# Performance work log

Hardware: AMD Instinct MI355X
Metric: run time of the kernel (lower is better)

## Reference

```python
import jax, jax.numpy as jnp
import numpy as np

B, S, HID = 2, 2048, 1024
H, KV, D = 16, 8, 64
NDIM = 2          # position_ids.shape[-1]
EPS = 1e-6
SCALING = 1.0


def _rms_norm(x, w=None, eps=EPS):
    # matches _RMSNorm: fp32 compute, optional learnable scale
    xf = x.astype(jnp.float32)
    n = xf * jax.lax.rsqrt(jnp.mean(xf * xf, axis=-1, keepdims=True) + eps)
    if w is not None:
        n = n * w.astype(jnp.float32)
    return n.astype(x.dtype)


def _rotate_half(x):
    d = x.shape[-1] // 2
    return jnp.concatenate([-x[..., d:], x[..., :d]], axis=-1)


def _apply_multidim_rope(x, cos, sin, ndim):
    # x: [B,S,h,D]; cos/sin: [B,S,D]; unsqueeze_dim=2 broadcasts over heads
    num_channels = x.shape[-1]
    cpd = 2 * (num_channels // (2 * ndim))  # channels per RoPE dimension
    outs = []
    for k in range(ndim):
        sl = slice(k * cpd, (k + 1) * cpd)
        xk = x[..., sl]
        ck = cos[..., sl][:, :, None, :]
        sk = sin[..., sl][:, :, None, :]
        outs.append(xk * ck + _rotate_half(xk) * sk)
    return jnp.concatenate(outs, axis=-1)


def setup_inputs() -> dict:
    key = jax.random.key(0)
    ks = jax.random.split(key, 10)
    scale = 0.02
    return {
        "hidden_states": jax.random.normal(ks[0], (B, S, HID), jnp.float32),
        "cos": jax.random.normal(ks[1], (B, S, D), jnp.float32),
        "sin": jax.random.normal(ks[2], (B, S, D), jnp.float32),
        "position_ids": jax.random.randint(ks[3], (B, S, NDIM), 0, 64, jnp.int64),
        "Wq": jax.random.normal(ks[4], (HID, H * D), jnp.float32) * scale,
        "Wk": jax.random.normal(ks[5], (HID, KV * D), jnp.float32) * scale,
        "Wv": jax.random.normal(ks[6], (HID, KV * D), jnp.float32) * scale,
        "Wo": jax.random.normal(ks[7], (H * D, HID), jnp.float32) * scale,
        "q_norm_w": jnp.ones((D,), jnp.float32),
        "k_norm_w": jnp.ones((D,), jnp.float32),
    }


def reference(hidden_states, cos, sin, position_ids, Wq, Wk, Wv, Wo, q_norm_w, k_norm_w):
    ndim = position_ids.shape[-1]
    bsz, seq_len, _ = hidden_states.shape

    q = (hidden_states @ Wq).reshape(bsz, seq_len, H, D)
    q = _rms_norm(q, q_norm_w)
    q = _apply_multidim_rope(q, cos, sin, ndim)
    q = jnp.transpose(q, (0, 2, 1, 3))  # [B,H,S,D]

    k = (hidden_states @ Wk).reshape(bsz, seq_len, KV, D)
    k = _rms_norm(k, k_norm_w)
    k = _apply_multidim_rope(k, cos, sin, ndim)
    k = jnp.transpose(k, (0, 2, 1, 3))  # [B,KV,S,D]

    v = (hidden_states @ Wv).reshape(bsz, seq_len, KV, D)
    v = _rms_norm(v, None)  # v_norm has no scale
    v = jnp.transpose(v, (0, 2, 1, 3))  # [B,KV,S,D]

    groups = H // KV
    if groups > 1:
        k = jnp.repeat(k, groups, axis=1)  # [B,H,S,D]
        v = jnp.repeat(v, groups, axis=1)

    scores = jnp.einsum("bhqd,bhkd->bhqk", q, k) * SCALING
    attn = jax.nn.softmax(scores.astype(jnp.float32), axis=-1).astype(q.dtype)
    out = jnp.einsum("bhqk,bhkd->bhqd", attn, v)
    out = jnp.transpose(out, (0, 2, 1, 3)).reshape(bsz, seq_len, H * D)
    return out @ Wo
```

## Files before the change

kernel.cpp:

```cpp
#include <hip/hip_runtime.h>

#define PB 2
#define PS 2048
#define PHID 1024
#define PH 16
#define PKV 8
#define PD 64
#define PM (PB*PS)
#define PR (PB*PH*PS)

typedef _Float16 f16_t;
typedef _Float16 f16x8 __attribute__((ext_vector_type(8)));
typedef _Float16 f16x2 __attribute__((ext_vector_type(2)));
typedef __fp16 fp16v2 __attribute__((ext_vector_type(2)));
typedef float f32x4 __attribute__((ext_vector_type(4)));

#define MFMAH(a,b,c)  __builtin_amdgcn_mfma_f32_16x16x32_f16((a),(b),(c),0,0,0)
#define LOG2E 1.44269504f

__device__ __forceinline__ void gl16(const f16_t* g, f16_t* l) {
  __builtin_amdgcn_global_load_lds(
      (const __attribute__((address_space(1))) void*)g,
      (__attribute__((address_space(3))) void*)l, 16, 0, 0);
}

__global__ __launch_bounds__(256)
void convert_all(const float* __restrict__ hs,
                 const float* __restrict__ Wq, const float* __restrict__ Wk,
                 const float* __restrict__ Wv, const float* __restrict__ Wo,
                 f16_t* __restrict__ hf, f16_t* __restrict__ wtT)
{
  __shared__ float Tt[64][68];
  const int tid = threadIdx.x;

  if (blockIdx.x < 2048) {
    const size_t i = ((size_t)blockIdx.x * 256 + tid) * 8;
    float4 a = *(const float4*)&hs[i];
    float4 b = *(const float4*)&hs[i + 4];
    float xs[8] = {a.x, a.y, a.z, a.w, b.x, b.y, b.z, b.w};
    f16x8 v;
    #pragma unroll
    for (int j = 0; j < 8; ++j) v[j] = (f16_t)xs[j];
    *(f16x8*)&hf[i] = v;
    return;
  }

  const int wb = blockIdx.x - 2048;
  const int slot = wb >> 4, k0 = (wb & 15) * 64;

  const float* src; int N, ncol0, orow0;
  if (slot < 16)      { src = Wq; N = 1024; ncol0 = slot*64;      orow0 = slot*64; }
  else if (slot < 24) { src = Wk; N = 512;  ncol0 = (slot-16)*64; orow0 = 1024 + (slot-16)*64; }
  else if (slot < 32) { src = Wv; N = 512;  ncol0 = (slot-24)*64; orow0 = 1536 + (slot-24)*64; }
  else                { src = Wo; N = 1024; ncol0 = (slot-32)*64; orow0 = 2048 + (slot-32)*64; }

  const int tk = tid >> 6, tn = tid & 63;
  #pragma unroll
  for (int i = 0; i < 16; ++i)
    Tt[tn][tk*16 + i] = src[(size_t)(k0 + tk*16 + i) * N + ncol0 + tn];
  __syncthreads();

  const int n = tid >> 2, kc = (tid & 3) * 16;
  f16x8 a0, a1;
  #pragma unroll
  for (int i = 0; i < 8; ++i) {
    a0[i] = (f16_t)Tt[n][kc + i];
    a1[i] = (f16_t)Tt[n][kc + 8 + i];
  }
  const size_t ob = (size_t)(orow0 + n) * 1024 + k0 + kc;
  *(f16x8*)&wtT[ob]     = a0;
  *(f16x8*)&wtT[ob + 8] = a1;
}

__global__ __launch_bounds__(256)
void qkv_kernel(const f16_t* __restrict__ hsf, const f16_t* __restrict__ wtT,
                const float* __restrict__ cosp, const float* __restrict__ sinp,
                const float* __restrict__ qnw, const float* __restrict__ knw,
                f16_t* __restrict__ q_o, f16_t* __restrict__ k_o,
                f16_t* __restrict__ vt_o)
{
  __shared__ __align__(16) f16_t Ah[128][64];
  __shared__ __align__(16) f16_t Bh[128][64];

  const int tid = threadIdx.x;
  const int lane = tid & 63, wave = tid >> 6;
  const int lo16 = lane & 15, hi4 = lane >> 4;
  const int lin = blockIdx.x;
  const int swz = (lin & 7) * 64 + (lin >> 3);
  const int m0 = (swz >> 4) * 128;
  const int ws = swz & 15;
  const int orow = ws * 128;

  int kind, hd0;
  if (ws < 8)       { kind = 0; hd0 = ws*2; }
  else if (ws < 12) { kind = 1; hd0 = (ws-8)*2; }
  else              { kind = 2; hd0 = (ws-12)*2; }

  f32x4 acc[2][8];
  #pragma unroll
  for (int qb = 0; qb < 2; ++qb)
    #pragma unroll
    for (int j = 0; j < 8; ++j) acc[qb][j] = f32x4{0.f, 0.f, 0.f, 0.f};

  const int ri = lane >> 3, pc = lane & 7;
  const int lcs = (pc ^ ri) * 8;
  size_t aoff4[4]; f16_t* aldst4[4];
  size_t boff4[4]; f16_t* bldst4[4];
  #pragma unroll
  for (int q = 0; q < 4; ++q) {
    aoff4[q] = (size_t)(m0 + wave*32 + q*8 + ri) * PHID + lcs;
    aldst4[q] = &Ah[wave*32 + q*8][0];
    boff4[q] = (size_t)(orow + wave*32 + q*8 + ri) * 1024 + lcs;
    bldst4[q] = &Bh[wave*32 + q*8][0];
  }

  const int rsw = lo16 & 7;

  for (int k0 = 0; k0 < PHID; k0 += 64) {
    __syncthreads();
    #pragma unroll
    for (int q = 0; q < 4; ++q) gl16(hsf + aoff4[q] + k0, aldst4[q]);
    #pragma unroll
    for (int q = 0; q < 4; ++q) gl16(wtT + boff4[q] + k0, bldst4[q]);
    __syncthreads();

    #pragma unroll
    for (int t = 0; t < 2; ++t) {
      const int ccol = ((t*4 + hi4) ^ rsw) * 8;
      f16x8 ah[2];
      #pragma unroll
      for (int qb = 0; qb < 2; ++qb)
        ah[qb] = *(const f16x8*)&Ah[wave*32 + qb*16 + lo16][ccol];
      #pragma unroll
      for (int j = 0; j < 8; ++j) {
        f16x8 bh = *(const f16x8*)&Bh[j*16 + lo16][ccol];
        #pragma unroll
        for (int qb = 0; qb < 2; ++qb)
          acc[qb][j] = MFMAH(ah[qb], bh, acc[qb][j]);
      }
    }
  }

  float nwv[4];
  #pragma unroll
  for (int jj = 0; jj < 4; ++jj)
    nwv[jj] = (kind == 0) ? qnw[lo16 + 16*jj]
            : (kind == 1) ? knw[lo16 + 16*jj] : 1.0f;

  #pragma unroll
  for (int qb = 0; qb < 2; ++qb) {
    float sc[2][4];
    #pragma unroll
    for (int r = 0; r < 4; ++r) {
      float s0 = 0.f, s1 = 0.f;
      #pragma unroll
      for (int j = 0; j < 4; ++j) {
        s0 += acc[qb][j][r]   * acc[qb][j][r];
        s1 += acc[qb][j+4][r] * acc[qb][j+4][r];
      }
      #pragma unroll
      for (int m = 1; m < 16; m <<= 1) {
        s0 += __shfl_xor(s0, m);
        s1 += __shfl_xor(s1, m);
      }
      sc[0][r] = 1.0f / sqrtf(s0 * (1.0f/64.0f) + 1e-6f);
      sc[1][r] = 1.0f / sqrtf(s1 * (1.0f/64.0f) + 1e-6f);
    }

    float y[8][4];
    #pragma unroll
    for (int j = 0; j < 8; ++j)
      #pragma unroll
      for (int r = 0; r < 4; ++r)
        y[j][r] = acc[qb][j][r] * sc[j>>2][r] * nwv[j&3];

    if (kind == 2) {
      #pragma unroll
      for (int r = 0; r < 4; ++r) {
        int mg = m0 + wave*32 + qb*16 + hi4*4 + r;
        int b = mg >> 11, sq = mg & 2047;
        int g = sq & 63;
        int sp = (g & 3) | (((g >> 4) & 1) << 2) | (((g >> 2) & 1) << 3)
               | (((g >> 3) & 1) << 4) | (g & 32);
        int sq2 = (sq & ~63) | sp;
        #pragma unroll
        for (int j = 0; j < 8; ++j) {
          int d = lo16 + 16*(j & 3), hd = hd0 + (j >> 2);
          vt_o[((size_t)((b*PKV + hd)*PD + d))*PS + sq2] = (f16_t)y[j][r];
        }
      }
    } else {
      #pragma unroll
      for (int r = 0; r < 4; ++r) {
        int mg = m0 + wave*32 + qb*16 + hi4*4 + r;
        int b = mg >> 11, sq = mg & 2047;
        const float* cp = &cosp[(size_t)mg * PD];
        const float* sp = &sinp[(size_t)mg * PD];
        float z[8];
        #pragma unroll
        for (int j = 0; j < 8; ++j) {
          int d = lo16 + 16*(j & 3);
          float c = cp[d], s = sp[d];
          float rot = (j & 1) ? y[j-1][r] : -y[j+1][r];
          z[j] = y[j][r] * c + rot * s;
        }
        #pragma unroll
        for (int j = 0; j < 8; ++j) {
          int d = lo16 + 16*(j & 3), hd = hd0 + (j >> 2);
          if (kind == 0) {
            size_t idx = ((size_t)(b*PH + hd)*PS + sq)*PD + d;
            q_o[idx] = (f16_t)(z[j] * LOG2E);
          } else {
            size_t idx = ((size_t)(b*PKV + hd)*PS + sq)*PD + d;
            k_o[idx] = (f16_t)z[j];
          }
        }
      }
    }
  }
}

__global__ __launch_bounds__(512, 4)
void attn_kernel(const f16_t* __restrict__ q_g, const f16_t* __restrict__ k_g,
                 const f16_t* __restrict__ vt_g,
                 f16_t* __restrict__ op, float2* __restrict__ ml)
{
  __shared__ __align__(16) char lds_raw[32768];
  f16_t (*Ks)[64][64] = (f16_t (*)[64][64])lds_raw;
  f16_t (*Vs)[64][64] = (f16_t (*)[64][64])(lds_raw + 16384);
  f16_t (*Ob)[72]     = (f16_t (*)[72])lds_raw;

  const int tid = threadIdx.x, lane = tid & 63, wave = tid >> 6;
  const int lo16 = lane & 15, hi4 = lane >> 4;
  const int lin = blockIdx.x;
  const int swz = (lin & 7) * 64 + (lin >> 3);
  const int qt = swz & 7;
  const int bh = (swz >> 3) & 31;
  const int ks = swz >> 8;
  const int b = bh >> 4, h = bh & 15, kvh = h >> 1;

  f16x8 qf[2][2];
  #pragma unroll
  for (int qb = 0; qb < 2; ++qb) {
    const size_t qbase = ((size_t)(b*PH + h)*PS + qt*256 + wave*32 + qb*16 + lo16) * PD;
    #pragma unroll
    for (int t = 0; t < 2; ++t)
      qf[qb][t] = *(const f16x8*)&q_g[qbase + t*32 + hi4*8];
  }

  f32x4 o[2][4];
  float mq[2] = {0.f, 0.f}, lq[2] = {0.f, 0.f};
  #pragma unroll
  for (int qb = 0; qb < 2; ++qb)
    #pragma unroll
    for (int j = 0; j < 4; ++j) o[qb][j] = f32x4{0.f, 0.f, 0.f, 0.f};

  const int ri = lane >> 3;
  const int lcs = ((lane & 7) ^ ri) * 8;
  const size_t kbase = (size_t)(b*PKV + kvh) * PS * PD + (size_t)ks * 1024 * PD;
  const size_t vbase = (size_t)(b*PKV + kvh) * PD * PS + (size_t)ks * 1024;

  auto STAGE = [&](int kt, int buf) {
    const f16_t* kp = k_g + kbase + (size_t)kt * 64 * PD;
    const f16_t* vp = vt_g + vbase + kt * 64;
    const int st = wave;
    gl16(kp + (st*8 + ri)*PD + lcs, &Ks[buf][st*8][0]);
    gl16(vp + (size_t)(st*8 + ri)*PS + lcs, &Vs[buf][st*8][0]);
  };

  STAGE(0, 0);
  int cur = 0;
  const int rsw = lo16 & 7;

  for (int kt = 0; kt < 16; ++kt) {
    __syncthreads();
    if (kt + 1 < 16) STAGE(kt + 1, cur ^ 1);

    f32x4 sacc[2][4];
    __builtin_amdgcn_s_setprio(1);
    #pragma unroll
    for (int j = 0; j < 4; ++j) {
      f16x8 kf0 = *(const f16x8*)&Ks[cur][j*16 + lo16][(hi4 ^ rsw) * 8];
      f16x8 kf1 = *(const f16x8*)&Ks[cur][j*16 + lo16][((4 + hi4) ^ rsw) * 8];
      #pragma unroll
      for (int qb = 0; qb < 2; ++qb) {
        const f32x4 mc = {-mq[qb], -mq[qb], -mq[qb], -mq[qb]};
        sacc[qb][j] = MFMAH(kf1, qf[qb][1], MFMAH(kf0, qf[qb][0], mc));
      }
    }
    __builtin_amdgcn_s_setprio(0);

    f16x8 pa[2][2];
    #pragma unroll
    for (int qb = 0; qb < 2; ++qb) {
      float x0 = fmaxf(fmaxf(sacc[qb][0][0], sacc[qb][0][1]),
                       fmaxf(sacc[qb][0][2], sacc[qb][0][3]));
      float x1 = fmaxf(fmaxf(sacc[qb][1][0], sacc[qb][1][1]),
                       fmaxf(sacc[qb][1][2], sacc[qb][1][3]));
      float x2 = fmaxf(fmaxf(sacc[qb][2][0], sacc[qb][2][1]),
                       fmaxf(sacc[qb][2][2], sacc[qb][2][3]));
      float x3 = fmaxf(fmaxf(sacc[qb][3][0], sacc[qb][3][1]),
                       fmaxf(sacc[qb][3][2], sacc[qb][3][3]));
      float tm = fmaxf(fmaxf(x0, x1), fmaxf(x2, x3));
      tm = fmaxf(tm, __shfl_xor(tm, 16));
      tm = fmaxf(tm, __shfl_xor(tm, 32));

      float ls = 0.f;
      if (!__all(tm <= 8.0f)) {
        float tmx = fmaxf(tm, 0.f);
        float alpha = __builtin_amdgcn_exp2f(-tmx);
        lq[qb] *= alpha;
        #pragma unroll
        for (int jd = 0; jd < 4; ++jd) o[qb][jd] *= alpha;
        mq[qb] += tmx;
        #pragma unroll
        for (int t = 0; t < 2; ++t) {
          union { fp16v2 h[4]; f16x8 v; } u;
          #pragma unroll
          for (int pr = 0; pr < 4; ++pr) {
            float p0 = __builtin_amdgcn_exp2f(sacc[qb][2*t + (pr>>1)][(pr&1)*2]     - tmx);
            float p1 = __builtin_amdgcn_exp2f(sacc[qb][2*t + (pr>>1)][(pr&1)*2 + 1] - tmx);
            ls += p0 + p1;
            u.h[pr] = __builtin_amdgcn_cvt_pkrtz(p0, p1);
          }
          pa[qb][t] = u.v;
        }
      } else {
        #pragma unroll
        for (int t = 0; t < 2; ++t) {
          union { fp16v2 h[4]; f16x8 v; } u;
          #pragma unroll
          for (int pr = 0; pr < 4; ++pr) {
            float p0 = __builtin_amdgcn_exp2f(sacc[qb][2*t + (pr>>1)][(pr&1)*2]);
            float p1 = __builtin_amdgcn_exp2f(sacc[qb][2*t + (pr>>1)][(pr&1)*2 + 1]);
            ls += p0 + p1;
            u.h[pr] = __builtin_amdgcn_cvt_pkrtz(p0, p1);
          }
          pa[qb][t] = u.v;
        }
      }
      lq[qb] += ls;
    }

    __builtin_amdgcn_s_setprio(1);
    #pragma unroll
    for (int jd = 0; jd < 4; ++jd) {
      #pragma unroll
      for (int t = 0; t < 2; ++t) {
        f16x8 vf = *(const f16x8*)&Vs[cur][jd*16 + lo16][((t*4 + hi4) ^ rsw) * 8];
        #pragma unroll
        for (int qb = 0; qb < 2; ++qb)
          o[qb][jd] = MFMAH(vf, pa[qb][t], o[qb][jd]);
      }
    }
    __builtin_amdgcn_s_setprio(0);

    cur ^= 1;
  }

  #pragma unroll
  for (int qb = 0; qb < 2; ++qb) {
    lq[qb] += __shfl_xor(lq[qb], 16);
    lq[qb] += __shfl_xor(lq[qb], 32);
  }
  __syncthreads();
  const int rbase = bh*PS + qt*256 + wave*32;
  if (hi4 == 0) {
    #pragma unroll
    for (int qb = 0; qb < 2; ++qb)
      ml[(size_t)ks*PR + rbase + qb*16 + lo16] = float2{mq[qb], lq[qb]};
  }
  const int wl = wave & 3;
  #pragma unroll
  for (int pass = 0; pass < 2; ++pass) {
    if ((wave >> 2) == pass) {
      #pragma unroll
      for (int qb = 0; qb < 2; ++qb) {
        float inv = 1.0f / lq[qb];
        #pragma unroll
        for (int jd = 0; jd < 4; ++jd)
          #pragma unroll
          for (int rp = 0; rp < 2; ++rp)
            *(f16x2*)&Ob[wl*32 + qb*16 + lo16][jd*16 + hi4*4 + 2*rp] =
                f16x2{(f16_t)(o[qb][jd][2*rp] * inv), (f16_t)(o[qb][jd][2*rp+1] * inv)};
      }
      const int row = lane >> 1, half = lane & 1;
      const size_t gb_ = ((size_t)ks*PR + rbase + row) * PD + half*32;
      #pragma unroll
      for (int c = 0; c < 4; ++c)
        *(f16x8*)&op[gb_ + c*8] = *(const f16x8*)&Ob[wl*32 + row][half*32 + c*8];
    }
    __syncthreads();
  }
}

__global__ __launch_bounds__(256)
void merge_kernel(const f16_t* __restrict__ op, const float2* __restrict__ ml,
                  f16_t* __restrict__ ao)
{
  const int gid = blockIdx.x * 256 + threadIdx.x;
  const int row = gid >> 3, oct = gid & 7;
  float2 e0 = ml[row], e1 = ml[PR + row];
  float M = fmaxf(e0.x, e1.x);
  float c0 = __builtin_amdgcn_exp2f(e0.x - M) * e0.y;
  float c1 = __builtin_amdgcn_exp2f(e1.x - M) * e1.y;
  float inv = 1.0f / (c0 + c1);
  c0 *= inv; c1 *= inv;
  f16x8 a = *(const f16x8*)&op[(size_t)row*PD + oct*8];
  f16x8 bq = *(const f16x8*)&op[(size_t)(PR + row)*PD + oct*8];
  f16x8 r;
  #pragma unroll
  for (int i = 0; i < 8; ++i)
    r[i] = (f16_t)(c0 * (float)a[i] + c1 * (float)bq[i]);
  const int bh = row >> 11, sq = row & 2047;
  const int b = bh >> 4, h = bh & 15;
  *(f16x8*)&ao[((size_t)(b*PS + sq))*PHID + h*PD + oct*8] = r;
}

__global__ __launch_bounds__(256)
void oproj_kernel(const f16_t* __restrict__ ao, const f16_t* __restrict__ woT,
                  float* __restrict__ out)
{
  __shared__ __align__(16) f16_t As[128][64];
  __shared__ __align__(16) f16_t Bs[64][64];

  const int tid = threadIdx.x;
  const int lane = tid & 63, wave = tid >> 6;
  const int lo16 = lane & 15, hi4 = lane >> 4;
  const int lin = blockIdx.x;
  const int swz = (lin & 7) * 64 + (lin >> 3);
  const int m0 = (swz >> 4) * 128;
  const int col0 = (swz & 15) * 64;

  f32x4 acc[2][4];
  #pragma unroll
  for (int qb = 0; qb < 2; ++qb)
    #pragma unroll
    for (int j = 0; j < 4; ++j) acc[qb][j] = f32x4{0.f, 0.f, 0.f, 0.f};

  const int ri = lane >> 3, pc = lane & 7;
  const int lcs = (pc ^ ri) * 8;
  size_t aoff4[4]; f16_t* aldst4[4];
  #pragma unroll
  for (int q = 0; q < 4; ++q) {
    aoff4[q] = (size_t)(m0 + wave*32 + q*8 + ri) * PHID + lcs;
    aldst4[q] = &As[wave*32 + q*8][0];
  }
  size_t boff[2]; int brow[2];
  #pragma unroll
  for (int q = 0; q < 2; ++q) {
    brow[q] = wave*16 + q*8;
    boff[q] = (size_t)(col0 + brow[q] + ri) * 1024 + lcs;
  }

  const int rsw = lo16 & 7;

  for (int k0 = 0; k0 < PHID; k0 += 64) {
    __syncthreads();
    #pragma unroll
    for (int q = 0; q < 4; ++q) gl16(ao + aoff4[q] + k0, aldst4[q]);
    #pragma unroll
    for (int q = 0; q < 2; ++q) gl16(woT + boff[q] + k0, &Bs[brow[q]][0]);
    __syncthreads();

    #pragma unroll
    for (int t = 0; t < 2; ++t) {
      const int ccol = ((t*4 + hi4) ^ rsw) * 8;
      f16x8 a[2];
      #pragma unroll
      for (int qb = 0; qb < 2; ++qb)
        a[qb] = *(const f16x8*)&As[wave*32 + qb*16 + lo16][ccol];
      #pragma unroll
      for (int j = 0; j < 4; ++j) {
        f16x8 bb = *(const f16x8*)&Bs[j*16 + lo16][ccol];
        #pragma unroll
        for (int qb = 0; qb < 2; ++qb)
          acc[qb][j] = MFMAH(a[qb], bb, acc[qb][j]);
      }
    }
  }

  #pragma unroll
  for (int qb = 0; qb < 2; ++qb)
    #pragma unroll
    for (int r = 0; r < 4; ++r) {
      int mg = m0 + wave*32 + qb*16 + hi4*4 + r;
      #pragma unroll
      for (int j = 0; j < 4; ++j)
        out[(size_t)mg*PHID + col0 + lo16 + 16*j] = acc[qb][j][r];
    }
}

extern "C" void kernel_launch(void* const* d_in, const int* in_sizes, int n_in,
                              void* d_out, int out_size, void* d_ws, size_t ws_size,
                              hipStream_t stream) {
  (void)in_sizes; (void)n_in; (void)out_size; (void)ws_size;
  const float* hs   = (const float*)d_in[0];
  const float* cosp = (const float*)d_in[1];
  const float* sinp = (const float*)d_in[2];
  const float* Wq   = (const float*)d_in[4];
  const float* Wk   = (const float*)d_in[5];
  const float* Wv   = (const float*)d_in[6];
  const float* Wo   = (const float*)d_in[7];
  const float* qnw  = (const float*)d_in[8];
  const float* knw  = (const float*)d_in[9];
  float* out = (float*)d_out;

  const size_t QN = (size_t)PB*PH*PS*PD;
  const size_t KN = (size_t)PB*PKV*PS*PD;
  const size_t HN = (size_t)PM*PHID;
  char* wsb = (char*)d_ws;
  f16_t*  qv  = (f16_t*)wsb;
  f16_t*  kv  = qv + QN;
  f16_t*  vt  = kv + KN;
  f16_t*  hsf = vt + KN;
  f16_t*  wtT = hsf + HN;
  f16_t*  op  = wtT + (size_t)3072*1024;
  float2* ml  = (float2*)(op + 2*QN);
  f16_t*  ao  = qv;
  const f16_t* woT = wtT + (size_t)2048*1024;

  convert_all<<<dim3(2816), 256, 0, stream>>>(hs, Wq, Wk, Wv, Wo, hsf, wtT);
  qkv_kernel<<<dim3(512),  256, 0, stream>>>(hsf, wtT, cosp, sinp,
                                             qnw, knw, qv, kv, vt);
  attn_kernel<<<dim3(512), 512, 0, stream>>>(qv, kv, vt, op, ml);
  merge_kernel<<<dim3(PR*8/256), 256, 0, stream>>>(op, ml, ao);
  oproj_kernel<<<dim3(512), 256, 0, stream>>>(ao, woT, out);
}
```

Baseline: 113.9 us.

## Fuse hidden-state fp16 conversion into QKV GEMM and split-merge into O-projection

The QKV GEMM now reads fp32 hidden states directly, converts them to fp16 in registers, and prefetches the next tile with register loads instead of using a separate conversion pass. The split-K attention merge is folded into the O-projection A-tile load, with a small kernel that precomputes only the per-row combine weights. This removes two full intermediate tensor round-trips through global memory and one kernel's worth of traffic. In exchange, the GEMM A loads become synchronous register loads plus conversion work, and oproj does redundant merge arithmetic across the 16 column blocks that share each row.

Result: slower. 135.3 us (+18.8%).

```diff
diff --git a/kernel.cpp b/kernel.cpp
--- a/kernel.cpp
+++ b/kernel.cpp
@@ -25,28 +25,13 @@
 }
 
 __global__ __launch_bounds__(256)
-void convert_all(const float* __restrict__ hs,
-                 const float* __restrict__ Wq, const float* __restrict__ Wk,
-                 const float* __restrict__ Wv, const float* __restrict__ Wo,
-                 f16_t* __restrict__ hf, f16_t* __restrict__ wtT)
+void convert_w(const float* __restrict__ Wq, const float* __restrict__ Wk,
+               const float* __restrict__ Wv, const float* __restrict__ Wo,
+               f16_t* __restrict__ wtT)
 {
   __shared__ float Tt[64][68];
   const int tid = threadIdx.x;
-
-  if (blockIdx.x < 2048) {
-    const size_t i = ((size_t)blockIdx.x * 256 + tid) * 8;
-    float4 a = *(const float4*)&hs[i];
-    float4 b = *(const float4*)&hs[i + 4];
-    float xs[8] = {a.x, a.y, a.z, a.w, b.x, b.y, b.z, b.w};
-    f16x8 v;
-    #pragma unroll
-    for (int j = 0; j < 8; ++j) v[j] = (f16_t)xs[j];
-    *(f16x8*)&hf[i] = v;
-    return;
-  }
-
-  const int wb = blockIdx.x - 2048;
-  const int slot = wb >> 4, k0 = (wb & 15) * 64;
+  const int slot = blockIdx.x >> 4, k0 = (blockIdx.x & 15) * 64;
 
   const float* src; int N, ncol0, orow0;
   if (slot < 16)      { src = Wq; N = 1024; ncol0 = slot*64;      orow0 = slot*64; }
@@ -73,7 +58,7 @@
 }
 
 __global__ __launch_bounds__(256)
-void qkv_kernel(const f16_t* __restrict__ hsf, const f16_t* __restrict__ wtT,
+void qkv_kernel(const float* __restrict__ hs, const f16_t* __restrict__ wtT,
                 const float* __restrict__ cosp, const float* __restrict__ sinp,
                 const float* __restrict__ qnw, const float* __restrict__ knw,
                 f16_t* __restrict__ q_o, f16_t* __restrict__ k_o,
@@ -103,25 +88,43 @@
     for (int j = 0; j < 8; ++j) acc[qb][j] = f32x4{0.f, 0.f, 0.f, 0.f};
 
   const int ri = lane >> 3, pc = lane & 7;
-  const int lcs = (pc ^ ri) * 8;
-  size_t aoff4[4]; f16_t* aldst4[4];
+  const int lc8 = (pc ^ ri) * 8;
+  size_t aoff4[4];
   size_t boff4[4]; f16_t* bldst4[4];
   #pragma unroll
   for (int q = 0; q < 4; ++q) {
-    aoff4[q] = (size_t)(m0 + wave*32 + q*8 + ri) * PHID + lcs;
-    aldst4[q] = &Ah[wave*32 + q*8][0];
-    boff4[q] = (size_t)(orow + wave*32 + q*8 + ri) * 1024 + lcs;
+    aoff4[q] = (size_t)(m0 + wave*32 + q*8 + ri) * PHID + lc8;
+    boff4[q] = (size_t)(orow + wave*32 + q*8 + ri) * 1024 + lc8;
     bldst4[q] = &Bh[wave*32 + q*8][0];
   }
 
   const int rsw = lo16 & 7;
+
+  float4 ga0[4], ga1[4];
+  auto LOADA = [&](int k0) {
+    #pragma unroll
+    for (int q = 0; q < 4; ++q) {
+      const float* p = hs + aoff4[q] + k0;
+      ga0[q] = *(const float4*)p;
+      ga1[q] = *(const float4*)(p + 4);
+    }
+  };
+  LOADA(0);
 
   for (int k0 = 0; k0 < PHID; k0 += 64) {
     __syncthreads();
     #pragma unroll
-    for (int q = 0; q < 4; ++q) gl16(hsf + aoff4[q] + k0, aldst4[q]);
+    for (int q = 0; q < 4; ++q) {
+      union { fp16v2 h[4]; f16x8 v; } u;
+      u.h[0] = __builtin_amdgcn_cvt_pkrtz(ga0[q].x, ga0[q].y);
+      u.h[1] = __builtin_amdgcn_cvt_pkrtz(ga0[q].z, ga0[q].w);
+      u.h[2] = __builtin_amdgcn_cvt_pkrtz(ga1[q].x, ga1[q].y);
+      u.h[3] = __builtin_amdgcn_cvt_pkrtz(ga1[q].z, ga1[q].w);
+      *(f16x8*)&Ah[wave*32 + q*8 + ri][pc*8] = u.v;
+    }
     #pragma unroll
     for (int q = 0; q < 4; ++q) gl16(wtT + boff4[q] + k0, bldst4[q]);
+    if (k0 + 64 < PHID) LOADA(k0 + 64);
     __syncthreads();
 
     #pragma unroll
@@ -395,31 +398,20 @@
 }
 
 __global__ __launch_bounds__(256)
-void merge_kernel(const f16_t* __restrict__ op, const float2* __restrict__ ml,
-                  f16_t* __restrict__ ao)
+void mlw_kernel(const float2* __restrict__ ml, float2* __restrict__ mw)
 {
-  const int gid = blockIdx.x * 256 + threadIdx.x;
-  const int row = gid >> 3, oct = gid & 7;
+  const int row = blockIdx.x * 256 + threadIdx.x;
   float2 e0 = ml[row], e1 = ml[PR + row];
   float M = fmaxf(e0.x, e1.x);
   float c0 = __builtin_amdgcn_exp2f(e0.x - M) * e0.y;
   float c1 = __builtin_amdgcn_exp2f(e1.x - M) * e1.y;
   float inv = 1.0f / (c0 + c1);
-  c0 *= inv; c1 *= inv;
-  f16x8 a = *(const f16x8*)&op[(size_t)row*PD + oct*8];
-  f16x8 bq = *(const f16x8*)&op[(size_t)(PR + row)*PD + oct*8];
-  f16x8 r;
-  #pragma unroll
-  for (int i = 0; i < 8; ++i)
-    r[i] = (f16_t)(c0 * (float)a[i] + c1 * (float)bq[i]);
-  const int bh = row >> 11, sq = row & 2047;
-  const int b = bh >> 4, h = bh & 15;
-  *(f16x8*)&ao[((size_t)(b*PS + sq))*PHID + h*PD + oct*8] = r;
+  mw[row] = float2{c0 * inv, c1 * inv};
 }
 
 __global__ __launch_bounds__(256)
-void oproj_kernel(const f16_t* __restrict__ ao, const f16_t* __restrict__ woT,
-                  float* __restrict__ out)
+void oproj_kernel(const f16_t* __restrict__ op, const float2* __restrict__ mw,
+                  const f16_t* __restrict__ woT, float* __restrict__ out)
 {
   __shared__ __align__(16) f16_t As[128][64];
   __shared__ __align__(16) f16_t Bs[64][64];
@@ -439,26 +431,46 @@
     for (int j = 0; j < 4; ++j) acc[qb][j] = f32x4{0.f, 0.f, 0.f, 0.f};
 
   const int ri = lane >> 3, pc = lane & 7;
-  const int lcs = (pc ^ ri) * 8;
-  size_t aoff4[4]; f16_t* aldst4[4];
+  const int lc8 = (pc ^ ri) * 8;
+
+  int bq_[4], sq_[4];
   #pragma unroll
   for (int q = 0; q < 4; ++q) {
-    aoff4[q] = (size_t)(m0 + wave*32 + q*8 + ri) * PHID + lcs;
-    aldst4[q] = &As[wave*32 + q*8][0];
-  }
+    int mg = m0 + wave*32 + q*8 + ri;
+    bq_[q] = mg >> 11; sq_[q] = mg & 2047;
+  }
+
   size_t boff[2]; int brow[2];
   #pragma unroll
   for (int q = 0; q < 2; ++q) {
     brow[q] = wave*16 + q*8;
-    boff[q] = (size_t)(col0 + brow[q] + ri) * 1024 + lcs;
+    boff[q] = (size_t)(col0 + brow[q] + ri) * 1024 + lc8;
   }
 
   const int rsw = lo16 & 7;
 
   for (int k0 = 0; k0 < PHID; k0 += 64) {
+    const int head = k0 >> 6;
+    f16x8 mval[4];
+    #pragma unroll
+    for (int q = 0; q < 4; ++q) {
+      const size_t opr = (size_t)((bq_[q]*PH + head))*PS + sq_[q];
+      f16x8 a0 = *(const f16x8*)&op[opr*PD + lc8];
+      f16x8 a1 = *(const f16x8*)&op[(PR + opr)*PD + lc8];
+      float2 w = mw[opr];
+      union { fp16v2 h[4]; f16x8 v; } u;
+      #pragma unroll
+      for (int e = 0; e < 4; ++e) {
+        float v0 = w.x * (float)a0[2*e]   + w.y * (float)a1[2*e];
+        float v1 = w.x * (float)a0[2*e+1] + w.y * (float)a1[2*e+1];
+        u.h[e] = __builtin_amdgcn_cvt_pkrtz(v0, v1);
+      }
+      mval[q] = u.v;
+    }
     __syncthreads();
     #pragma unroll
-    for (int q = 0; q < 4; ++q) gl16(ao + aoff4[q] + k0, aldst4[q]);
+    for (int q = 0; q < 4; ++q)
+      *(f16x8*)&As[wave*32 + q*8 + ri][pc*8] = mval[q];
     #pragma unroll
     for (int q = 0; q < 2; ++q) gl16(woT + boff[q] + k0, &Bs[brow[q]][0]);
     __syncthreads();
@@ -508,22 +520,20 @@
 
   const size_t QN = (size_t)PB*PH*PS*PD;
   const size_t KN = (size_t)PB*PKV*PS*PD;
-  const size_t HN = (size_t)PM*PHID;
   char* wsb = (char*)d_ws;
   f16_t*  qv  = (f16_t*)wsb;
   f16_t*  kv  = qv + QN;
   f16_t*  vt  = kv + KN;
-  f16_t*  hsf = vt + KN;
-  f16_t*  wtT = hsf + HN;
+  f16_t*  wtT = vt + KN;
   f16_t*  op  = wtT + (size_t)3072*1024;
   float2* ml  = (float2*)(op + 2*QN);
-  f16_t*  ao  = qv;
+  float2* mw  = ml + 2*(size_t)PR;
   const f16_t* woT = wtT + (size_t)2048*1024;
 
-  convert_all<<<dim3(2816), 256, 0, stream>>>(hs, Wq, Wk, Wv, Wo, hsf, wtT);
-  qkv_kernel<<<dim3(512),  256, 0, stream>>>(hsf, wtT, cosp, sinp,
-                                             qnw, knw, qv, kv, vt);
+  convert_w<<<dim3(768),  256, 0, stream>>>(Wq, Wk, Wv, Wo, wtT);
+  qkv_kernel<<<dim3(512), 256, 0, stream>>>(hs, wtT, cosp, sinp,
+                                            qnw, knw, qv, kv, vt);
   attn_kernel<<<dim3(512), 512, 0, stream>>>(qv, kv, vt, op, ml);
-  merge_kernel<<<dim3(PR*8/256), 256, 0, stream>>>(op, ml, ao);
-  oproj_kernel<<<dim3(512), 256, 0, stream>>>(ao, woT, out);
-}
+  mlw_kernel<<<dim3(PR/256), 256, 0, stream>>>(ml, mw);
+  oproj_kernel<<<dim3(512), 256, 0, stream>>>(op, mw, woT, out);
+}
```
